# Performance work log

Measured on AMD Instinct MI355X. Metric: run time of the kernel, lower is better.

The kernel has to match this reference:

```python
import jax, jax.numpy as jnp
import numpy as np
import math

PATCH = 9
C_IN = 128
C_FEAT = 128
B, H, W = 32, 96, 96


def setup_inputs() -> dict:
    key = jax.random.key(0)
    k1, k2, k3 = jax.random.split(key, 3)
    input1 = jax.random.normal(k1, (B, C_IN, H, W), dtype=jnp.float32)
    input2 = jax.random.normal(k2, (B, C_IN, H, W), dtype=jnp.float32)
    # 1x1 conv params (kernel_size=1 -> weight is effectively [C_out, C_in])
    proj_w = jax.random.normal(k3, (C_FEAT, C_IN), dtype=jnp.float32) / math.sqrt(C_IN)
    proj_b = jnp.zeros((C_FEAT,), dtype=jnp.float32)
    return {"input1": input1, "input2": input2, "proj_w": proj_w, "proj_b": proj_b}


def _proj(x, w, b):
    # 1x1 conv == per-pixel channel mixing
    return jnp.einsum('bchw,fc->bfhw', x, w) + b[None, :, None, None]


def reference(input1, input2, proj_w, proj_b):
    x1 = _proj(input1, proj_w, proj_b)          # [B, F, H, W]
    x2 = _proj(input2, proj_w, proj_b)          # [B, F, H, W]
    r = PATCH // 2
    h, w = x1.shape[-2:]
    x2p = jnp.pad(x2, ((0, 0), (0, 0), (r, r), (r, r)))  # zero-pad borders
    # Cost volume: for each displacement (di, dj) in the PATCH x PATCH window,
    # sum over channels of x1[.,.,i,j] * x2[.,.,i+di-r, j+dj-r].
    corrs = []
    for di in range(PATCH):
        for dj in range(PATCH):
            shifted = x2p[:, :, di:di + h, dj:dj + w]
            corrs.append(jnp.einsum('bchw,bchw->bhw', x1, shifted))
    out = jnp.stack(corrs, axis=1)              # [B, PATCH*PATCH, H, W]
    return out / math.sqrt(C_FEAT)
```

## Files before the change

### kernel.cpp

```cpp
#include <hip/hip_runtime.h>
#include <stdint.h>

#define B_   32
#define CIN  128
#define HH   96
#define WW   96
#define HW   (HH*WW)
#define NPIX (B_*HW)
#define AROWS 144
#define APAD  136
#define SCALE 0.08838834764831845f
#define ESW   100

#define AB_OFF 0u
#define V_OFF  36864u
#define S_OFF  37376u
#define Y2_OFF 40960u
#define Z2_OFF (Y2_OFF + 75497472u)
#define ZP_OFF (Z2_OFF + 1179648u)
#define WS_NEED (ZP_OFF + 16384u)

typedef __attribute__((ext_vector_type(8))) short bf16x8;
typedef __attribute__((ext_vector_type(4))) float f32x4;

__device__ inline unsigned short f2bf(float f) {
    unsigned int u = __float_as_uint(f);
    u += 0x7fffu + ((u >> 16) & 1u);
    return (unsigned short)(u >> 16);
}

__device__ inline int bswz(int row, int byteoff) {
    return row * 128 + (byteoff ^ (((row ^ (row >> 3)) & 7) << 4));
}

__global__ __launch_bounds__(128) void k1_prep(
    const float* __restrict__ Wm, const float* __restrict__ bias,
    unsigned short* __restrict__ Abuf, float* __restrict__ vbuf,
    float* __restrict__ sbuf, char* __restrict__ zp) {
    int r = blockIdx.x;
    int c = threadIdx.x;
    int gid = r * 128 + c;
    if (gid < 1024)
        *(uint4*)(zp + gid * 16) = make_uint4(0u, 0u, 0u, 0u);

    float acc = 0.f;
    if (r < 128) {
        for (int f = 0; f < 128; ++f)
            acc += Wm[f * 128 + r] * Wm[f * 128 + c];
    } else if (r == 128) {
        for (int f = 0; f < 128; ++f)
            acc += Wm[f * 128 + c] * bias[f];
        vbuf[c] = acc;
        if (c == 0) {
            float s = 0.f;
            for (int f = 0; f < 128; ++f) s += bias[f] * bias[f];
            sbuf[0] = s;
        }
    }
    Abuf[r * 128 + c] = f2bf(acc);
}

__global__ __launch_bounds__(512, 4) void k2_proj(
    const float* __restrict__ a2, const unsigned short* __restrict__ Abuf,
    const float* __restrict__ vbuf, const float* __restrict__ sbuf,
    unsigned short* __restrict__ y2, float* __restrict__ z2) {
    __shared__ __align__(16) unsigned short Asm[AROWS * APAD];
    __shared__ __align__(128) unsigned char Bsm[2][128 * 128];

    const int t = threadIdx.x;
    const int tile = blockIdx.x;
    const int b = tile / 72;
    const int hw0 = (tile - b * 72) * 128;

    for (int i = t; i < 2304; i += 512) {
        int row = i >> 4, seg = i & 15;
        *(uint4*)(&Asm[row * APAD + seg * 8]) =
            *(const uint4*)(Abuf + row * 128 + seg * 8);
    }

    {
        const int pxq = t & 31;
        const int ctp = t >> 5;
        const float* a2b = a2 + (size_t)b * (CIN * HW) + hw0 + pxq * 4;
#pragma unroll
        for (int it = 0; it < 4; ++it) {
            const int cc0 = (ctp + it * 16) * 2;
            float4 f0 = *(const float4*)(a2b + (size_t)cc0 * HW);
            float4 f1 = *(const float4*)(a2b + (size_t)(cc0 + 1) * HW);
            unsigned char* pl = Bsm[cc0 >> 6];
            const int bo = (cc0 & 63) * 2;
            float a0[4] = {f0.x, f0.y, f0.z, f0.w};
            float a1[4] = {f1.x, f1.y, f1.z, f1.w};
#pragma unroll
            for (int r = 0; r < 4; ++r) {
                unsigned int pk = (unsigned int)f2bf(a0[r]) |
                                  ((unsigned int)f2bf(a1[r]) << 16);
                *(unsigned int*)(&pl[bswz(pxq * 4 + r, bo)]) = pk;
            }
        }
    }
    __syncthreads();

    const int wv = t >> 6;
    const int l = t & 63;
    const int li = l & 15;
    const int hi = l >> 4;
    const int rbase = hi * 4;
    const int pxl = wv * 16 + li;

    bf16x8 bfr[4];
#pragma unroll
    for (int kk = 0; kk < 4; ++kk) {
        const int k0 = kk * 32 + hi * 8;
        bfr[kk] = *(const bf16x8*)(&Bsm[k0 >> 6][bswz(pxl, (k0 & 63) * 2)]);
    }

    f32x4 acc[9];
#pragma unroll
    for (int m = 0; m < 9; ++m) acc[m] = (f32x4){0.f, 0.f, 0.f, 0.f};

#pragma unroll
    for (int kk = 0; kk < 4; ++kk) {
        const int k0 = kk * 32 + hi * 8;
#pragma unroll
        for (int m = 0; m < 9; ++m) {
            bf16x8 af = *(const bf16x8*)(&Asm[(m * 16 + li) * APAD + k0]);
            acc[m] = __builtin_amdgcn_mfma_f32_16x16x32_bf16(af, bfr[kk], acc[m], 0, 0, 0);
        }
    }

    const int px = hw0 + pxl;
    const size_t pxoff = (size_t)b * HW + px;
#pragma unroll
    for (int m = 0; m < 8; ++m) {
        int c0 = m * 16 + rbase;
        ushort4 pk;
        pk.x = f2bf(acc[m].x + vbuf[c0 + 0]);
        pk.y = f2bf(acc[m].y + vbuf[c0 + 1]);
        pk.z = f2bf(acc[m].z + vbuf[c0 + 2]);
        pk.w = f2bf(acc[m].w + vbuf[c0 + 3]);
        *(ushort4*)(y2 + ((size_t)(c0 >> 3) * NPIX + pxoff) * 8 + (c0 & 7)) = pk;
    }
    if (rbase == 0) {
        z2[pxoff] = acc[8].x + sbuf[0];
    }
}

__global__ __launch_bounds__(256, 3) void k3_corr(
    const float* __restrict__ x1, const char* __restrict__ wsb,
    const float* __restrict__ z2, float* __restrict__ out) {
    __shared__ float Zs[9 * 104];
    __shared__ __align__(128) unsigned char EX[32512];
    float* Es = (float*)EX;

    const int t = threadIdx.x;
    const int bx = blockIdx.x;
    const int b = blockIdx.y;
    const int h = (bx & 7) * 12 + (bx >> 3);

    const int wv = t >> 6;
    const int l = t & 63;
    const int li = l & 15;
    const int hi = l >> 4;

    for (int cell = t; cell < 936; cell += 256) {
        int r = cell / 104, sx = cell - r * 104;
        int hs = h - 4 + r, wsx = sx - 4;
        float zv = 0.f;
        if ((unsigned)hs < 96u && (unsigned)wsx < 96u)
            zv = z2[(size_t)b * HW + hs * 96 + wsx];
        Zs[cell] = zv;
    }

    if (t < 128) {
        int pl = t >> 6, r = (t >> 3) & 7, sgm = t & 7;
        *(uint4*)(&EX[pl * 13312 + (96 + r) * 128 + sgm * 16]) =
            make_uint4(0u, 0u, 0u, 0u);
    }
    {
        const float* x1b = x1 + (size_t)b * (CIN * HW) + (size_t)h * 96;
#pragma unroll
        for (int it = 0; it < 6; ++it) {
            int idx = t + it * 256;
            int ccp = idx / 24;
            int pxq = idx - ccp * 24;
            int cc0 = ccp * 2;
            float4 f0 = *(const float4*)(x1b + (size_t)cc0 * HW + pxq * 4);
            float4 f1 = *(const float4*)(x1b + (size_t)(cc0 + 1) * HW + pxq * 4);
            unsigned char* pl = EX + (cc0 >> 6) * 13312;
            const int bo = (cc0 & 63) * 2;
            float a0[4] = {f0.x, f0.y, f0.z, f0.w};
            float a1[4] = {f1.x, f1.y, f1.z, f1.w};
#pragma unroll
            for (int r = 0; r < 4; ++r) {
                unsigned int pk = (unsigned int)f2bf(a0[r]) |
                                  ((unsigned int)f2bf(a1[r]) << 16);
                *(unsigned int*)(&pl[bswz(pxq * 4 + r, bo)]) = pk;
            }
        }
    }

    unsigned offb[12];
#pragma unroll
    for (int cc = 0; cc < 4; ++cc)
#pragma unroll
        for (int g = 0; g < 3; ++g) {
            const int pxj = (wv * 3 + g) * 8 + li - 4;
            long off;
            if ((unsigned)pxj < 96u)
                off = (long)Y2_OFF +
                      ((long)(cc * 4 + hi) * NPIX + (long)b * HW +
                       (long)(h - 4) * 96 + pxj) * 16;
            else
                off = (long)ZP_OFF;
            offb[cc * 3 + g] = (unsigned)off;
        }

    __syncthreads();

    bf16x8 afr[3][4];
#pragma unroll
    for (int g = 0; g < 3; ++g) {
        const int px = (wv * 3 + g) * 8 + li;
#pragma unroll
        for (int cc = 0; cc < 4; ++cc) {
            const int k0 = cc * 32 + hi * 8;
            afr[g][cc] = *(const bf16x8*)(
                &EX[(k0 >> 6) * 13312 + bswz(px, (k0 & 63) * 2)]);
        }
    }
    __syncthreads();

    uint4 pvA[2][6], pvB[2][6];
#pragma unroll
    for (int q = 0; q < 6; ++q)
        pvA[0][q] = *(const uint4*)(wsb + offb[q]);
#pragma unroll
    for (int q = 0; q < 6; ++q)
        pvB[0][q] = *(const uint4*)(wsb + offb[6 + q]);

#pragma unroll
    for (int di = 0; di < 9; ++di) {
        const int cur = di & 1, nxt = cur ^ 1;
        if (di < 8) {
#pragma unroll
            for (int q = 0; q < 6; ++q)
                pvA[nxt][q] = *(const uint4*)(wsb + offb[q] + (di + 1) * 1536);
        }

        const int hs = h - 4 + di;
        f32x4 ac[3];
#pragma unroll
        for (int g = 0; g < 3; ++g) ac[g] = (f32x4){0.f, 0.f, 0.f, 0.f};

        if ((unsigned)hs < 96u) {
#pragma unroll
            for (int cc = 0; cc < 4; ++cc)
#pragma unroll
                for (int g = 0; g < 3; ++g) {
                    union { uint4 u; bf16x8 f; } cv;
                    cv.u = (cc < 2) ? pvA[cur][cc * 3 + g]
                                    : pvB[cur][(cc - 2) * 3 + g];
                    ac[g] = __builtin_amdgcn_mfma_f32_16x16x32_bf16(
                        afr[g][cc], cv.f, ac[g], 0, 0, 0);
                }
        }

        if (l < 32) {
#pragma unroll
            for (int g = 0; g < 3; ++g) {
                const int uu = wv * 3 + g;
                const float zv = Zs[di * 104 + uu * 8 + li];
#pragma unroll
                for (int reg = 0; reg < 4; ++reg) {
                    const int i = hi * 4 + reg;
                    const int dji = li - i;
                    if (dji >= 0 && dji <= 8)
                        Es[(di * 9 + dji) * ESW + uu * 8 + i] =
                            (ac[g][reg] + zv) * SCALE;
                }
            }
        }

        if (di < 8) {
#pragma unroll
            for (int q = 0; q < 6; ++q)
                pvB[nxt][q] = *(const uint4*)(wsb + offb[6 + q] + (di + 1) * 1536);
        }
    }

    __syncthreads();
    const size_t ob = (size_t)b * 81 * HW + (size_t)h * 96;
    for (int idx = t; idx < 81 * 96; idx += 256) {
        int s = idx / 96, w = idx - s * 96;
        out[ob + (size_t)s * HW + w] = Es[s * ESW + w];
    }
}

extern "C" void kernel_launch(void* const* d_in, const int* in_sizes, int n_in,
                              void* d_out, int out_size, void* d_ws, size_t ws_size,
                              hipStream_t stream) {
    const float* input1 = (const float*)d_in[0];
    const float* input2 = (const float*)d_in[1];
    const float* proj_w = (const float*)d_in[2];
    const float* proj_b = (const float*)d_in[3];
    float* out = (float*)d_out;

    char* ws = (char*)d_ws;
    if (ws_size < WS_NEED) return;

    unsigned short* Abuf = (unsigned short*)(ws + AB_OFF);
    float* vbuf = (float*)(ws + V_OFF);
    float* sbuf = (float*)(ws + S_OFF);
    unsigned short* y2 = (unsigned short*)(ws + Y2_OFF);
    float* z2 = (float*)(ws + Z2_OFF);
    char* zp = ws + ZP_OFF;

    k1_prep<<<dim3(144), dim3(128), 0, stream>>>(proj_w, proj_b, Abuf, vbuf, sbuf, zp);
    k2_proj<<<dim3(2304), dim3(512), 0, stream>>>(input2, Abuf, vbuf, sbuf, y2, z2);
    k3_corr<<<dim3(96, 32), dim3(256), 0, stream>>>(input1, ws, z2, out);
}
```

Measured before the change: 183.4 us.

## Process two output rows per block in correlation kernel to reuse shifted y2 loads

```diff
diff --git a/kernel.cpp b/kernel.cpp
--- a/kernel.cpp
+++ b/kernel.cpp
@@ -10,7 +10,7 @@
 #define AROWS 144
 #define APAD  136
 #define SCALE 0.08838834764831845f
-#define ESW   100
+#define ESW   97
 
 #define AB_OFF 0u
 #define V_OFF  36864u
@@ -146,56 +146,45 @@
     }
 }
 
-__global__ __launch_bounds__(256, 3) void k3_corr(
+__global__ __launch_bounds__(256, 2) void k3_corr(
     const float* __restrict__ x1, const char* __restrict__ wsb,
-    const float* __restrict__ z2, float* __restrict__ out) {
-    __shared__ float Zs[9 * 104];
-    __shared__ __align__(128) unsigned char EX[32512];
+    float* __restrict__ out) {
+    __shared__ __align__(128) unsigned char EX[62880];
     float* Es = (float*)EX;
 
     const int t = threadIdx.x;
     const int bx = blockIdx.x;
     const int b = blockIdx.y;
-    const int h = (bx & 7) * 12 + (bx >> 3);
+    const int h = ((bx & 7) * 6 + (bx >> 3)) * 2;
 
     const int wv = t >> 6;
     const int l = t & 63;
     const int li = l & 15;
     const int hi = l >> 4;
 
-    for (int cell = t; cell < 936; cell += 256) {
-        int r = cell / 104, sx = cell - r * 104;
-        int hs = h - 4 + r, wsx = sx - 4;
-        float zv = 0.f;
-        if ((unsigned)hs < 96u && (unsigned)wsx < 96u)
-            zv = z2[(size_t)b * HW + hs * 96 + wsx];
-        Zs[cell] = zv;
-    }
-
-    if (t < 128) {
-        int pl = t >> 6, r = (t >> 3) & 7, sgm = t & 7;
-        *(uint4*)(&EX[pl * 13312 + (96 + r) * 128 + sgm * 16]) =
-            make_uint4(0u, 0u, 0u, 0u);
-    }
     {
         const float* x1b = x1 + (size_t)b * (CIN * HW) + (size_t)h * 96;
 #pragma unroll
-        for (int it = 0; it < 6; ++it) {
-            int idx = t + it * 256;
-            int ccp = idx / 24;
-            int pxq = idx - ccp * 24;
-            int cc0 = ccp * 2;
-            float4 f0 = *(const float4*)(x1b + (size_t)cc0 * HW + pxq * 4);
-            float4 f1 = *(const float4*)(x1b + (size_t)(cc0 + 1) * HW + pxq * 4);
-            unsigned char* pl = EX + (cc0 >> 6) * 13312;
-            const int bo = (cc0 & 63) * 2;
-            float a0[4] = {f0.x, f0.y, f0.z, f0.w};
-            float a1[4] = {f1.x, f1.y, f1.z, f1.w};
-#pragma unroll
-            for (int r = 0; r < 4; ++r) {
-                unsigned int pk = (unsigned int)f2bf(a0[r]) |
-                                  ((unsigned int)f2bf(a1[r]) << 16);
-                *(unsigned int*)(&pl[bswz(pxq * 4 + r, bo)]) = pk;
+        for (int im = 0; im < 2; ++im) {
+            const float* xr = x1b + im * 96;
+#pragma unroll
+            for (int it = 0; it < 6; ++it) {
+                int idx = t + it * 256;
+                int ccp = idx / 24;
+                int pxq = idx - ccp * 24;
+                int cc0 = ccp * 2;
+                float4 f0 = *(const float4*)(xr + (size_t)cc0 * HW + pxq * 4);
+                float4 f1 = *(const float4*)(xr + (size_t)(cc0 + 1) * HW + pxq * 4);
+                unsigned char* pl = EX + im * 24576 + (cc0 >> 6) * 12288;
+                const int bo = (cc0 & 63) * 2;
+                float a0[4] = {f0.x, f0.y, f0.z, f0.w};
+                float a1[4] = {f1.x, f1.y, f1.z, f1.w};
+#pragma unroll
+                for (int r = 0; r < 4; ++r) {
+                    unsigned int pk = (unsigned int)f2bf(a0[r]) |
+                                      ((unsigned int)f2bf(a1[r]) << 16);
+                    *(unsigned int*)(&pl[bswz(pxq * 4 + r, bo)]) = pk;
+                }
             }
         }
     }
@@ -216,17 +205,30 @@
             offb[cc * 3 + g] = (unsigned)off;
         }
 
+    int offz[3];
+#pragma unroll
+    for (int g = 0; g < 3; ++g) {
+        const int zc = (wv * 3 + g) * 8 + li - 4;
+        offz[g] = ((unsigned)zc < 96u)
+            ? (int)Z2_OFF + (b * HW + (h - 4) * 96 + zc) * 4
+            : (int)ZP_OFF;
+    }
+
     __syncthreads();
 
     bf16x8 afr[3][4];
-#pragma unroll
-    for (int g = 0; g < 3; ++g) {
-        const int px = (wv * 3 + g) * 8 + li;
-#pragma unroll
-        for (int cc = 0; cc < 4; ++cc) {
-            const int k0 = cc * 32 + hi * 8;
-            afr[g][cc] = *(const bf16x8*)(
-                &EX[(k0 >> 6) * 13312 + bswz(px, (k0 & 63) * 2)]);
+    {
+        const int imA = li >> 3;
+        const int pA = li & 7;
+#pragma unroll
+        for (int g = 0; g < 3; ++g) {
+            const int px = (wv * 3 + g) * 8 + pA;
+#pragma unroll
+            for (int cc = 0; cc < 4; ++cc) {
+                const int k0 = cc * 32 + hi * 8;
+                afr[g][cc] = *(const bf16x8*)(
+                    &EX[imA * 24576 + (k0 >> 6) * 12288 + bswz(px, (k0 & 63) * 2)]);
+            }
         }
     }
     __syncthreads();
@@ -240,20 +242,27 @@
         pvB[0][q] = *(const uint4*)(wsb + offb[6 + q]);
 
 #pragma unroll
-    for (int di = 0; di < 9; ++di) {
+    for (int di = 0; di < 10; ++di) {
         const int cur = di & 1, nxt = cur ^ 1;
-        if (di < 8) {
+        if (di < 9) {
 #pragma unroll
             for (int q = 0; q < 6; ++q)
                 pvA[nxt][q] = *(const uint4*)(wsb + offb[q] + (di + 1) * 1536);
         }
 
         const int hs = h - 4 + di;
+        const int zrowok = ((unsigned)hs < 96u);
+        float zv[3];
+#pragma unroll
+        for (int g = 0; g < 3; ++g)
+            zv[g] = *(const float*)(wsb + (zrowok ? offz[g] + di * 384
+                                                  : (int)ZP_OFF));
+
         f32x4 ac[3];
 #pragma unroll
         for (int g = 0; g < 3; ++g) ac[g] = (f32x4){0.f, 0.f, 0.f, 0.f};
 
-        if ((unsigned)hs < 96u) {
+        if (zrowok) {
 #pragma unroll
             for (int cc = 0; cc < 4; ++cc)
 #pragma unroll
@@ -266,23 +275,26 @@
                 }
         }
 
-        if (l < 32) {
-#pragma unroll
-            for (int g = 0; g < 3; ++g) {
-                const int uu = wv * 3 + g;
-                const float zv = Zs[di * 104 + uu * 8 + li];
-#pragma unroll
-                for (int reg = 0; reg < 4; ++reg) {
-                    const int i = hi * 4 + reg;
-                    const int dji = li - i;
-                    if (dji >= 0 && dji <= 8)
-                        Es[(di * 9 + dji) * ESW + uu * 8 + i] =
-                            (ac[g][reg] + zv) * SCALE;
+        {
+            const int imw = hi >> 1;
+            const int rnd = di - imw;
+            if ((unsigned)rnd < 9u) {
+#pragma unroll
+                for (int g = 0; g < 3; ++g) {
+                    const int uu = wv * 3 + g;
+#pragma unroll
+                    for (int reg = 0; reg < 4; ++reg) {
+                        const int ip = (hi & 1) * 4 + reg;
+                        const int dji = li - ip;
+                        if (dji >= 0 && dji <= 8)
+                            Es[(imw * 81 + rnd * 9 + dji) * ESW + uu * 8 + ip] =
+                                (ac[g][reg] + zv[g]) * SCALE;
+                    }
                 }
             }
         }
 
-        if (di < 8) {
+        if (di < 9) {
 #pragma unroll
             for (int q = 0; q < 6; ++q)
                 pvB[nxt][q] = *(const uint4*)(wsb + offb[6 + q] + (di + 1) * 1536);
@@ -291,9 +303,11 @@
 
     __syncthreads();
     const size_t ob = (size_t)b * 81 * HW + (size_t)h * 96;
-    for (int idx = t; idx < 81 * 96; idx += 256) {
-        int s = idx / 96, w = idx - s * 96;
-        out[ob + (size_t)s * HW + w] = Es[s * ESW + w];
+    for (int idx = t; idx < 2 * 81 * 96; idx += 256) {
+        int p = idx / (81 * 96);
+        int r2 = idx - p * (81 * 96);
+        int s = r2 / 96, w = r2 - s * 96;
+        out[ob + (size_t)s * HW + p * 96 + w] = Es[(p * 81 + s) * ESW + w];
     }
 }
 
@@ -318,5 +332,5 @@
 
     k1_prep<<<dim3(144), dim3(128), 0, stream>>>(proj_w, proj_b, Abuf, vbuf, sbuf, zp);
     k2_proj<<<dim3(2304), dim3(512), 0, stream>>>(input2, Abuf, vbuf, sbuf, y2, z2);
-    k3_corr<<<dim3(96, 32), dim3(256), 0, stream>>>(input1, ws, z2, out);
-}
+    k3_corr<<<dim3(48, 32), dim3(256), 0, stream>>>(input1, ws, out);
+}
```

New measurement: 169.5 us. 7.6% less time.
